# Optimization experiments

Hardware: AMD Instinct MI355X
Metric: run time of the kernel (lower is better)

The kernel has to match this reference:

```python
import jax, jax.numpy as jnp
import numpy as np

N_ = 50000   # nodes
E_ = 800000  # edges
G_ = 64      # graphs in batch
EPS = 1e-5   # batchnorm eps


def _lin(k, fi, fo):
    s = 1.0 / np.sqrt(fi)
    return jax.random.uniform(k, (fi, fo), jnp.float32, -s, s)


def setup_inputs() -> dict:
    key = jax.random.key(0)
    ks = jax.random.split(key, 16)
    d_in, d_h, d_out = 128, 128, 5000
    inp = {
        'x': jax.random.normal(ks[0], (N_, d_in), jnp.float32),
        'edge_index': jax.random.randint(ks[1], (2, E_), 0, N_, jnp.int32),
        'batch': jnp.sort(jax.random.randint(ks[2], (N_,), 0, G_, jnp.int32)),
    }
    dims = [(d_in, d_h), (d_h, d_h), (d_h, d_h), (d_h, d_h)]
    for i, (fi, fo) in enumerate(dims, 1):
        inp[f'w{i}'] = _lin(ks[2 + i], fi, fo)
        inp[f'b{i}'] = jnp.zeros((fo,), jnp.float32)
        inp[f'g{i}'] = jnp.ones((fo,), jnp.float32)   # BN gamma
        inp[f'be{i}'] = jnp.zeros((fo,), jnp.float32)  # BN beta
    inp['gw1'] = _lin(ks[7], d_h, d_h // 2)
    inp['gb1'] = jnp.zeros((d_h // 2,), jnp.float32)
    inp['gw2'] = _lin(ks[8], d_h // 2, 1)
    inp['gb2'] = jnp.zeros((1,), jnp.float32)
    inp['cw'] = _lin(ks[9], d_h, d_out)
    inp['cb'] = jnp.zeros((d_out,), jnp.float32)
    return inp


def reference(x, w1, b1, g1, be1, w2, b2, g2, be2, w3, b3, g3, be3,
              w4, b4, g4, be4, gw1, gb1, gw2, gb2, cw, cb,
              edge_index, batch):
    # GCN normalization with self-loops (PyG GCNConv semantics)
    loops = jnp.arange(N_, dtype=edge_index.dtype)
    src = jnp.concatenate([edge_index[0], loops])
    dst = jnp.concatenate([edge_index[1], loops])
    deg = jax.ops.segment_sum(jnp.ones(src.shape[0], jnp.float32), dst, N_)
    dis = jax.lax.rsqrt(jnp.maximum(deg, 1.0))  # deg >= 1 with self-loops
    norm = dis[src] * dis[dst]                  # [E+N]

    def gcn(h, w, b):
        hw = h @ w                              # [N, d]
        msg = hw[src] * norm[:, None]           # gather over edges
        return jax.ops.segment_sum(msg, dst, N_) + b

    def bn(h, g, be):
        m = h.mean(0)
        v = h.var(0)                            # biased var (training BN)
        return (h - m) * jax.lax.rsqrt(v + EPS) * g + be

    h = x
    for w, b, g, be in ((w1, b1, g1, be1), (w2, b2, g2, be2),
                        (w3, b3, g3, be3), (w4, b4, g4, be4)):
        h = jax.nn.relu(bn(gcn(h, w, b), g, be))  # dropout is identity (eval)

    # attention pooling: per-graph softmax over gate scores
    gate = jax.nn.relu(h @ gw1 + gb1) @ gw2 + gb2  # [N, 1]
    gate = gate[:, 0]
    m = jax.ops.segment_max(gate, batch, G_)
    e = jnp.exp(gate - m[batch])
    s = jax.ops.segment_sum(e, batch, G_)
    a = e / s[batch]                               # [N]
    pooled = jax.ops.segment_sum(h * a[:, None], batch, G_)  # [G, d]
    return pooled @ cw + cb                        # [G, out]
```

## Files before the change

kernel.cpp:

```cpp
#include <hip/hip_runtime.h>
#include <hip/hip_bf16.h>
#include <hip/hip_fp16.h>

#define NN   50000
#define NE   800000
#define NG   64
#define DH   128
#define DOUT 5000
#define BNEPS 1e-5f
#define NBLK 196

typedef _Float16 h8 __attribute__((ext_vector_type(8)));
typedef float    f4 __attribute__((ext_vector_type(4)));

__global__ __launch_bounds__(256) void k_count(const int* __restrict__ dst, int* __restrict__ cnt) {
    int e = blockIdx.x * 256 + threadIdx.x;
    if (e < NE) atomicAdd(&cnt[dst[e]], 1);
}

__global__ __launch_bounds__(256) void k_blkscan(const int* __restrict__ cnt, int* __restrict__ rowptr,
                                                 int* __restrict__ bsum) {
    __shared__ int s[256];
    int t = threadIdx.x, i = blockIdx.x * 256 + t;
    int v = (i < NN) ? cnt[i] : 0;
    s[t] = v;
    __syncthreads();
    for (int off = 1; off < 256; off <<= 1) {
        int x = (t >= off) ? s[t - off] : 0;
        __syncthreads();
        s[t] += x;
        __syncthreads();
    }
    if (i < NN) rowptr[i] = s[t] - v;
    if (t == 255) bsum[blockIdx.x] = s[255];
}

__global__ __launch_bounds__(256) void k_bscan(const int* __restrict__ bsum, int* __restrict__ boff) {
    __shared__ int s[256];
    int t = threadIdx.x;
    int v = (t < NBLK) ? bsum[t] : 0;
    s[t] = v;
    __syncthreads();
    for (int off = 1; off < 256; off <<= 1) {
        int x = (t >= off) ? s[t - off] : 0;
        __syncthreads();
        s[t] += x;
        __syncthreads();
    }
    if (t < NBLK) boff[t] = s[t] - v;
}

__global__ __launch_bounds__(256) void k_fin(int* __restrict__ rowptr, const int* __restrict__ boff,
                                             int* __restrict__ cnt, float* __restrict__ dis) {
    int i = blockIdx.x * 256 + threadIdx.x;
    if (i >= NN) { if (i == NN) rowptr[NN] = NE; return; }
    rowptr[i] += boff[blockIdx.x];
    dis[i] = rsqrtf((float)(cnt[i] + 1));
    cnt[i] = 0;
}

__global__ __launch_bounds__(256) void k_fill(const int* __restrict__ ei, const int* __restrict__ rowptr,
                                              int* __restrict__ fil, const float* __restrict__ dis,
                                              int2* __restrict__ ew) {
    int e = blockIdx.x * 256 + threadIdx.x;
    if (e >= NE) return;
    int s = ei[e], d = ei[NE + e];
    int p = rowptr[d] + atomicAdd(&fil[d], 1);
    ew[p] = make_int2(s, __float_as_int(dis[s] * dis[d]));
}

__global__ __launch_bounds__(256) void k_wprep(const float* __restrict__ W0, const float* __restrict__ W1,
                                               const float* __restrict__ W2, const float* __restrict__ W3,
                                               const float* __restrict__ GW1, __half* __restrict__ Wt) {
    const float* Ws[5] = {W0, W1, W2, W3, GW1};
    int m = blockIdx.x >> 4;
    int chunk = blockIdx.x & 15;
    const float* W = Ws[m];
    __half* O = Wt + m * DH * DH;
    int ncol = (m == 4) ? 64 : DH;
    int total = ncol * DH;
    int o = chunk * 1024 + threadIdx.x;
    for (int r = 0; r < 4; r++, o += 256) {
        if (o < total) {
            int c = o >> 7, k = o & 127;
            O[o] = __float2half(W[k * ncol + c]);
        }
    }
}

__global__ __launch_bounds__(256) void k_gemm3(const float* __restrict__ X, const __half* __restrict__ Wt,
                                               const float* __restrict__ scale, const float* __restrict__ shift,
                                               __half* __restrict__ Y) {
    int t = threadIdx.x;
    int lane = t & 63, wid = t >> 6;
    int wr = wid >> 1, wc = wid & 1;
    int row0 = blockIdx.x * 64;
    int lr = lane & 15, lk = (lane >> 4) * 8;

    f4 acc[2][4];
#pragma unroll
    for (int i = 0; i < 2; i++)
#pragma unroll
        for (int j = 0; j < 4; j++) acc[i][j] = (f4){0.f, 0.f, 0.f, 0.f};

    for (int kt = 0; kt < 4; kt++) {
        int kbase = kt * 32 + lk;
        h8 afr[2];
#pragma unroll
        for (int fr = 0; fr < 2; fr++) {
            int gr = row0 + wr * 32 + fr * 16 + lr;
            gr = min(gr, NN - 1);
            const float4* p = (const float4*)(X + (size_t)gr * DH + kbase);
            float4 v0 = p[0], v1 = p[1];
            if (scale) {
                const float4* sc4 = (const float4*)(scale + kbase);
                const float4* sh4 = (const float4*)(shift + kbase);
                float4 s0 = sc4[0], s1 = sc4[1], h0 = sh4[0], h1 = sh4[1];
                v0.x = fmaxf(fmaf(v0.x, s0.x, h0.x), 0.f);
                v0.y = fmaxf(fmaf(v0.y, s0.y, h0.y), 0.f);
                v0.z = fmaxf(fmaf(v0.z, s0.z, h0.z), 0.f);
                v0.w = fmaxf(fmaf(v0.w, s0.w, h0.w), 0.f);
                v1.x = fmaxf(fmaf(v1.x, s1.x, h1.x), 0.f);
                v1.y = fmaxf(fmaf(v1.y, s1.y, h1.y), 0.f);
                v1.z = fmaxf(fmaf(v1.z, s1.z, h1.z), 0.f);
                v1.w = fmaxf(fmaf(v1.w, s1.w, h1.w), 0.f);
            }
            h8 a;
            a[0] = (_Float16)v0.x; a[1] = (_Float16)v0.y; a[2] = (_Float16)v0.z; a[3] = (_Float16)v0.w;
            a[4] = (_Float16)v1.x; a[5] = (_Float16)v1.y; a[6] = (_Float16)v1.z; a[7] = (_Float16)v1.w;
            afr[fr] = a;
        }
#pragma unroll
        for (int fc = 0; fc < 4; fc++) {
            int gc = wc * 64 + fc * 16 + lr;
            h8 b = *(const h8*)(Wt + (size_t)gc * DH + kbase);
#pragma unroll
            for (int fr = 0; fr < 2; fr++)
                acc[fr][fc] = __builtin_amdgcn_mfma_f32_16x16x32_f16(afr[fr], b, acc[fr][fc], 0, 0, 0);
        }
    }
#pragma unroll
    for (int fr = 0; fr < 2; fr++) {
#pragma unroll
        for (int fc = 0; fc < 4; fc++) {
            int C = wc * 64 + fc * 16 + lr;
#pragma unroll
            for (int q = 0; q < 4; q++) {
                int R = row0 + wr * 32 + fr * 16 + (lane >> 4) * 4 + q;
                if (R < NN) Y[(size_t)R * DH + C] = __float2half(acc[fr][fc][q]);
            }
        }
    }
}

#define EDGE(e) { int2 r = HW4[(size_t)(e).x * 32 + sl]; \
                  float w = __int_as_float((e).y); \
                  float2 g0 = __half22float2(*(__half2*)&r.x), g1 = __half22float2(*(__half2*)&r.y); \
                  a0 = fmaf(w, g0.x, a0); a1 = fmaf(w, g0.y, a1); \
                  a2 = fmaf(w, g1.x, a2); a3 = fmaf(w, g1.y, a3); }

__global__ __launch_bounds__(256) void k_agg(const __half* __restrict__ HW, const int* __restrict__ rowptr,
                                             const int2* __restrict__ EW, const float* __restrict__ dis,
                                             float* __restrict__ OUT,
                                             float* __restrict__ ssum, float* __restrict__ ssq) {
    __shared__ float lsum[DH], lsq[DH];
    int t = threadIdx.x;
    if (t < DH) { lsum[t] = 0.f; lsq[t] = 0.f; }
    __syncthreads();
    int wid = t >> 6, lane = t & 63;
    int sub = lane >> 5, sl = lane & 31;
    const int2* HW4 = (const int2*)HW;
    float4* OUT4 = (float4*)OUT;
    float s0 = 0, s1 = 0, s2 = 0, s3 = 0, q0 = 0, q1 = 0, q2 = 0, q3 = 0;
    int gw = blockIdx.x * 4 + wid;
    for (int i = gw * 2 + sub; i < NN; i += 16384) {
        float sd = dis[i];
        int2 hr = HW4[(size_t)i * 32 + sl];
        float2 f0 = __half22float2(*(__half2*)&hr.x);
        float2 f1 = __half22float2(*(__half2*)&hr.y);
        float wslf = sd * sd;
        float a0 = wslf * f0.x, a1 = wslf * f0.y;
        float a2 = wslf * f1.x, a3 = wslf * f1.y;
        int p = rowptr[i], p1 = rowptr[i + 1];
        for (; p + 8 <= p1; p += 8) {
            int2 e0 = EW[p], e1 = EW[p + 1], e2 = EW[p + 2], e3 = EW[p + 3];
            int2 e4 = EW[p + 4], e5 = EW[p + 5], e6 = EW[p + 6], e7 = EW[p + 7];
            EDGE(e0) EDGE(e1) EDGE(e2) EDGE(e3)
            EDGE(e4) EDGE(e5) EDGE(e6) EDGE(e7)
        }
        if (p + 4 <= p1) {
            int2 e0 = EW[p], e1 = EW[p + 1], e2 = EW[p + 2], e3 = EW[p + 3];
            EDGE(e0) EDGE(e1) EDGE(e2) EDGE(e3)
            p += 4;
        }
        for (; p < p1; p++) {
            int2 e = EW[p];
            EDGE(e)
        }
        OUT4[(size_t)i * 32 + sl] = make_float4(a0, a1, a2, a3);
        s0 += a0; s1 += a1; s2 += a2; s3 += a3;
        q0 += a0 * a0; q1 += a1 * a1; q2 += a2 * a2; q3 += a3 * a3;
    }
    atomicAdd(&lsum[sl * 4 + 0], s0); atomicAdd(&lsum[sl * 4 + 1], s1);
    atomicAdd(&lsum[sl * 4 + 2], s2); atomicAdd(&lsum[sl * 4 + 3], s3);
    atomicAdd(&lsq[sl * 4 + 0], q0);  atomicAdd(&lsq[sl * 4 + 1], q1);
    atomicAdd(&lsq[sl * 4 + 2], q2);  atomicAdd(&lsq[sl * 4 + 3], q3);
    __syncthreads();
    if (t < DH) { atomicAdd(&ssum[t], lsum[t]); atomicAdd(&ssq[t], lsq[t]); }
}

__global__ void k_bnfin(float* __restrict__ ssum, float* __restrict__ ssq,
                        const float* __restrict__ g, const float* __restrict__ be,
                        float* __restrict__ scale, float* __restrict__ shift) {
    int f = threadIdx.x;
    float m = ssum[f] * (1.f / NN);
    float v = ssq[f] * (1.f / NN) - m * m;
    float r = rsqrtf(v + BNEPS);
    float sc = r * g[f];
    scale[f] = sc;
    shift[f] = fmaf(-m, sc, be[f]);
    ssum[f] = 0.f;
    ssq[f] = 0.f;
}

__global__ __launch_bounds__(256) void k_gateM(const float* __restrict__ H, const float* __restrict__ scale,
                                               const float* __restrict__ shift, const __half* __restrict__ gw1t,
                                               const float* __restrict__ gb1, const float* __restrict__ gw2,
                                               const float* __restrict__ gb2, float* __restrict__ gate) {
    int t = threadIdx.x, lane = t & 63, w = t >> 6;
    int row0 = blockIdx.x * 64 + w * 16;
    int lr = lane & 15, lk = (lane >> 4) * 8;
    f4 acc[4];
#pragma unroll
    for (int fc = 0; fc < 4; fc++) acc[fc] = (f4){0.f, 0.f, 0.f, 0.f};

    for (int kt = 0; kt < 4; kt++) {
        int kbase = kt * 32 + lk;
        int gr = min(row0 + lr, NN - 1);
        const float4* p = (const float4*)(H + (size_t)gr * DH + kbase);
        float4 v0 = p[0], v1 = p[1];
        const float4* sc4 = (const float4*)(scale + kbase);
        const float4* sh4 = (const float4*)(shift + kbase);
        float4 s0 = sc4[0], s1 = sc4[1], h0 = sh4[0], h1 = sh4[1];
        v0.x = fmaxf(fmaf(v0.x, s0.x, h0.x), 0.f);
        v0.y = fmaxf(fmaf(v0.y, s0.y, h0.y), 0.f);
        v0.z = fmaxf(fmaf(v0.z, s0.z, h0.z), 0.f);
        v0.w = fmaxf(fmaf(v0.w, s0.w, h0.w), 0.f);
        v1.x = fmaxf(fmaf(v1.x, s1.x, h1.x), 0.f);
        v1.y = fmaxf(fmaf(v1.y, s1.y, h1.y), 0.f);
        v1.z = fmaxf(fmaf(v1.z, s1.z, h1.z), 0.f);
        v1.w = fmaxf(fmaf(v1.w, s1.w, h1.w), 0.f);
        h8 a;
        a[0] = (_Float16)v0.x; a[1] = (_Float16)v0.y; a[2] = (_Float16)v0.z; a[3] = (_Float16)v0.w;
        a[4] = (_Float16)v1.x; a[5] = (_Float16)v1.y; a[6] = (_Float16)v1.z; a[7] = (_Float16)v1.w;
#pragma unroll
        for (int fc = 0; fc < 4; fc++) {
            h8 b = *(const h8*)(gw1t + (size_t)(fc * 16 + lr) * DH + kbase);
            acc[fc] = __builtin_amdgcn_mfma_f32_16x16x32_f16(a, b, acc[fc], 0, 0, 0);
        }
    }
    float vq[4] = {0.f, 0.f, 0.f, 0.f};
#pragma unroll
    for (int fc = 0; fc < 4; fc++) {
        float b1 = gb1[fc * 16 + lr];
        float w2 = gw2[fc * 16 + lr];
#pragma unroll
        for (int q = 0; q < 4; q++)
            vq[q] = fmaf(fmaxf(acc[fc][q] + b1, 0.f), w2, vq[q]);
    }
#pragma unroll
    for (int m = 1; m < 16; m <<= 1) {
#pragma unroll
        for (int q = 0; q < 4; q++) vq[q] += __shfl_xor(vq[q], m, 64);
    }
    if (lr == 0) {
        float b2 = gb2[0];
        int rbase = row0 + (lane >> 4) * 4;
#pragma unroll
        for (int q = 0; q < 4; q++)
            if (rbase + q < NN) gate[rbase + q] = vq[q] + b2;
    }
}

__device__ __forceinline__ int lbound(const int* __restrict__ a, int v) {
    int lo = 0, hi = NN;
    while (lo < hi) {
        int mid = (lo + hi) >> 1;
        if (a[mid] < v) lo = mid + 1; else hi = mid;
    }
    return lo;
}

__global__ __launch_bounds__(256) void k_pms(const float* __restrict__ gate, const int* __restrict__ batch,
                                             float* __restrict__ ms, float* __restrict__ pooled) {
    __shared__ float red[256];
    int g = blockIdx.x, t = threadIdx.x;
    if (t < DH) pooled[g * DH + t] = 0.f;
    int s = lbound(batch, g), e = lbound(batch, g + 1);
    float m = -INFINITY;
    for (int i = s + t; i < e; i += 256) m = fmaxf(m, gate[i]);
    red[t] = m; __syncthreads();
    for (int off = 128; off > 0; off >>= 1) { if (t < off) red[t] = fmaxf(red[t], red[t + off]); __syncthreads(); }
    m = red[0];
    __syncthreads();
    float se = 0.f;
    for (int i = s + t; i < e; i += 256) se += __expf(gate[i] - m);
    red[t] = se; __syncthreads();
    for (int off = 128; off > 0; off >>= 1) { if (t < off) red[t] += red[t + off]; __syncthreads(); }
    if (t == 0) {
        ms[g * 2] = m;
        ms[g * 2 + 1] = (e > s) ? 1.f / red[0] : 0.f;
    }
}

#define PNODES 8
__global__ __launch_bounds__(256) void k_pool2(const float* __restrict__ H, const float* __restrict__ scale,
                                               const float* __restrict__ shift, const float* __restrict__ gate,
                                               const int* __restrict__ batch, const float* __restrict__ ms,
                                               float* __restrict__ pooled) {
    int wid = threadIdx.x >> 6, lane = threadIdx.x & 63;
    int base = (blockIdx.x * 4 + wid) * PNODES;
    if (base >= NN) return;
    int end = min(base + PNODES, NN);
    const float2* H2 = (const float2*)H;
    float2 sc2 = ((const float2*)scale)[lane];
    float2 sh2 = ((const float2*)shift)[lane];
    float2 acc = make_float2(0.f, 0.f);
    int curg = batch[base];
    for (int i = base; i < end; i++) {
        int g = batch[i];
        if (g != curg) {
            atomicAdd(&pooled[curg * DH + lane * 2], acc.x);
            atomicAdd(&pooled[curg * DH + lane * 2 + 1], acc.y);
            acc = make_float2(0.f, 0.f);
            curg = g;
        }
        float a = __expf(gate[i] - ms[g * 2]) * ms[g * 2 + 1];
        float2 h = H2[(size_t)i * 64 + lane];
        float hx = fmaxf(fmaf(h.x, sc2.x, sh2.x), 0.f);
        float hy = fmaxf(fmaf(h.y, sc2.y, sh2.y), 0.f);
        acc.x = fmaf(a, hx, acc.x);
        acc.y = fmaf(a, hy, acc.y);
    }
    atomicAdd(&pooled[curg * DH + lane * 2], acc.x);
    atomicAdd(&pooled[curg * DH + lane * 2 + 1], acc.y);
}

__global__ __launch_bounds__(256) void k_cls(const float* __restrict__ pooled, const float* __restrict__ cw,
                                             const float* __restrict__ cb, float* __restrict__ out) {
    __shared__ float pr[DH];
    int g = blockIdx.y;
    if (threadIdx.x < DH) pr[threadIdx.x] = pooled[g * DH + threadIdx.x];
    __syncthreads();
    int j = blockIdx.x * 256 + threadIdx.x;
    if (j >= DOUT) return;
    float acc = cb[j];
#pragma unroll 8
    for (int k = 0; k < DH; k++) acc = fmaf(pr[k], cw[k * DOUT + j], acc);
    out[g * DOUT + j] = acc;
}

extern "C" void kernel_launch(void* const* d_in, const int* in_sizes, int n_in,
                              void* d_out, int out_size, void* d_ws, size_t ws_size,
                              hipStream_t stream) {
    const float* x     = (const float*)d_in[0];
    const int*   ei    = (const int*)d_in[1];
    const int*   batch = (const int*)d_in[2];
    const float* w[4]  = {(const float*)d_in[3], (const float*)d_in[7], (const float*)d_in[11], (const float*)d_in[15]};
    const float* gg[4] = {(const float*)d_in[5], (const float*)d_in[9], (const float*)d_in[13], (const float*)d_in[17]};
    const float* be[4] = {(const float*)d_in[6], (const float*)d_in[10], (const float*)d_in[14], (const float*)d_in[18]};
    const float* gw1 = (const float*)d_in[19];
    const float* gb1 = (const float*)d_in[20];
    const float* gw2 = (const float*)d_in[21];
    const float* gb2 = (const float*)d_in[22];
    const float* cw  = (const float*)d_in[23];
    const float* cb  = (const float*)d_in[24];

    char* base = (char*)d_ws;
    size_t off = 0;
    auto take = [&](size_t n) -> char* { char* r = base + off; off = (off + n + 255) & ~(size_t)255; return r; };
    float*  bufA   = (float*)take((size_t)NN * DH * 4);
    __half* bufB   = (__half*)take((size_t)NN * DH * 2);
    int2*  ew     = (int2*)take((size_t)NE * 8);
    int*   rowptr = (int*)take((size_t)(NN + 1) * 4);
    int*   cnt    = (int*)take((size_t)NN * 4);
    float* dis    = (float*)take((size_t)NN * 4);
    float* gate   = (float*)take((size_t)NN * 4);
    float* stats  = (float*)take(2 * DH * 4);
    float* ssum = stats, *ssq = stats + DH;
    float* scale  = (float*)take(DH * 4);
    float* shift  = (float*)take(DH * 4);
    float* pooled = (float*)take((size_t)NG * DH * 4);
    int*   bsum   = (int*)take((size_t)256 * 4);
    int*   boff   = (int*)take((size_t)256 * 4);
    float* ms     = (float*)take((size_t)NG * 2 * 4);
    __half* Wt    = (__half*)take((size_t)5 * DH * DH * 2);
    __half* gw1t  = Wt + (size_t)4 * DH * DH;

    hipMemsetAsync(cnt, 0, NN * 4, stream);
    hipMemsetAsync(stats, 0, 2 * DH * 4, stream);
    k_count<<<(NE + 255) / 256, 256, 0, stream>>>(ei + NE, cnt);
    k_blkscan<<<NBLK, 256, 0, stream>>>(cnt, rowptr, bsum);
    k_bscan<<<1, 256, 0, stream>>>(bsum, boff);
    k_fin<<<NBLK, 256, 0, stream>>>(rowptr, boff, cnt, dis);
    k_fill<<<(NE + 255) / 256, 256, 0, stream>>>(ei, rowptr, cnt, dis, ew);
    k_wprep<<<72, 256, 0, stream>>>(w[0], w[1], w[2], w[3], gw1, Wt);

    const int gemm_grid = (NN + 63) / 64;
    for (int L = 0; L < 4; L++) {
        k_gemm3<<<gemm_grid, 256, 0, stream>>>(L == 0 ? x : bufA, Wt + (size_t)L * DH * DH,
                                               L == 0 ? nullptr : scale,
                                               L == 0 ? nullptr : shift, bufB);
        k_agg<<<2048, 256, 0, stream>>>(bufB, rowptr, ew, dis, bufA, ssum, ssq);
        k_bnfin<<<1, DH, 0, stream>>>(ssum, ssq, gg[L], be[L], scale, shift);
    }
    k_gateM<<<(NN + 63) / 64, 256, 0, stream>>>(bufA, scale, shift, gw1t, gb1, gw2, gb2, gate);
    k_pms<<<NG, 256, 0, stream>>>(gate, batch, ms, pooled);
    k_pool2<<<(NN + 4 * PNODES - 1) / (4 * PNODES), 256, 0, stream>>>(bufA, scale, shift, gate, batch, ms, pooled);
    k_cls<<<dim3((DOUT + 255) / 256, NG), 256, 0, stream>>>(pooled, cw, cb, (float*)d_out);
}
```

Baseline: 584.3 us.

## Store aggregated activations in fp16 and fold BN finalize into aggregation kernel

The aggregation output buffer changes from fp32 to fp16, halving the bytes written by k_agg and read by the next layer's GEMM, gate and pooling kernels. The separate one-block BN finalize kernel is removed: the last aggregation block, found with an atomic ticket, computes scale and shift and resets the accumulators. The two memsets are merged into one. This saves launches and memory traffic but adds fp16 rounding of pre-BN activations and a fence-plus-ticket pattern that must be correct.

```diff
diff --git a/kernel.cpp b/kernel.cpp
--- a/kernel.cpp
+++ b/kernel.cpp
@@ -9,6 +9,7 @@
 #define DOUT 5000
 #define BNEPS 1e-5f
 #define NBLK 196
+#define AGG_GRID 2048
 
 typedef _Float16 h8 __attribute__((ext_vector_type(8)));
 typedef float    f4 __attribute__((ext_vector_type(4)));
@@ -88,7 +89,8 @@
     }
 }
 
-__global__ __launch_bounds__(256) void k_gemm3(const float* __restrict__ X, const __half* __restrict__ Wt,
+__global__ __launch_bounds__(256) void k_gemm3(const float* __restrict__ Xf, const __half* __restrict__ Xh,
+                                               const __half* __restrict__ Wt,
                                                const float* __restrict__ scale, const float* __restrict__ shift,
                                                __half* __restrict__ Y) {
     int t = threadIdx.x;
@@ -110,24 +112,31 @@
         for (int fr = 0; fr < 2; fr++) {
             int gr = row0 + wr * 32 + fr * 16 + lr;
             gr = min(gr, NN - 1);
-            const float4* p = (const float4*)(X + (size_t)gr * DH + kbase);
-            float4 v0 = p[0], v1 = p[1];
-            if (scale) {
+            float fv[8];
+            if (Xf) {
+                const float4* p = (const float4*)(Xf + (size_t)gr * DH + kbase);
+                float4 v0 = p[0], v1 = p[1];
+                fv[0] = v0.x; fv[1] = v0.y; fv[2] = v0.z; fv[3] = v0.w;
+                fv[4] = v1.x; fv[5] = v1.y; fv[6] = v1.z; fv[7] = v1.w;
+            } else {
+                int4 hv = *(const int4*)(Xh + (size_t)gr * DH + kbase);
+                float2 p0 = __half22float2(*(__half2*)&hv.x);
+                float2 p1 = __half22float2(*(__half2*)&hv.y);
+                float2 p2 = __half22float2(*(__half2*)&hv.z);
+                float2 p3 = __half22float2(*(__half2*)&hv.w);
+                fv[0] = p0.x; fv[1] = p0.y; fv[2] = p1.x; fv[3] = p1.y;
+                fv[4] = p2.x; fv[5] = p2.y; fv[6] = p3.x; fv[7] = p3.y;
                 const float4* sc4 = (const float4*)(scale + kbase);
                 const float4* sh4 = (const float4*)(shift + kbase);
                 float4 s0 = sc4[0], s1 = sc4[1], h0 = sh4[0], h1 = sh4[1];
-                v0.x = fmaxf(fmaf(v0.x, s0.x, h0.x), 0.f);
-                v0.y = fmaxf(fmaf(v0.y, s0.y, h0.y), 0.f);
-                v0.z = fmaxf(fmaf(v0.z, s0.z, h0.z), 0.f);
-                v0.w = fmaxf(fmaf(v0.w, s0.w, h0.w), 0.f);
-                v1.x = fmaxf(fmaf(v1.x, s1.x, h1.x), 0.f);
-                v1.y = fmaxf(fmaf(v1.y, s1.y, h1.y), 0.f);
-                v1.z = fmaxf(fmaf(v1.z, s1.z, h1.z), 0.f);
-                v1.w = fmaxf(fmaf(v1.w, s1.w, h1.w), 0.f);
+                float sv[8] = {s0.x, s0.y, s0.z, s0.w, s1.x, s1.y, s1.z, s1.w};
+                float hv2[8] = {h0.x, h0.y, h0.z, h0.w, h1.x, h1.y, h1.z, h1.w};
+#pragma unroll
+                for (int j = 0; j < 8; j++) fv[j] = fmaxf(fmaf(fv[j], sv[j], hv2[j]), 0.f);
             }
             h8 a;
-            a[0] = (_Float16)v0.x; a[1] = (_Float16)v0.y; a[2] = (_Float16)v0.z; a[3] = (_Float16)v0.w;
-            a[4] = (_Float16)v1.x; a[5] = (_Float16)v1.y; a[6] = (_Float16)v1.z; a[7] = (_Float16)v1.w;
+#pragma unroll
+            for (int j = 0; j < 8; j++) a[j] = (_Float16)fv[j];
             afr[fr] = a;
         }
 #pragma unroll
@@ -161,8 +170,11 @@
 
 __global__ __launch_bounds__(256) void k_agg(const __half* __restrict__ HW, const int* __restrict__ rowptr,
                                              const int2* __restrict__ EW, const float* __restrict__ dis,
-                                             float* __restrict__ OUT,
-                                             float* __restrict__ ssum, float* __restrict__ ssq) {
+                                             __half* __restrict__ OUT,
+                                             float* __restrict__ ssum, float* __restrict__ ssq,
+                                             const float* __restrict__ gg, const float* __restrict__ be,
+                                             float* __restrict__ scale, float* __restrict__ shift,
+                                             int* __restrict__ ticket) {
     __shared__ float lsum[DH], lsq[DH];
     int t = threadIdx.x;
     if (t < DH) { lsum[t] = 0.f; lsq[t] = 0.f; }
@@ -170,7 +182,6 @@
     int wid = t >> 6, lane = t & 63;
     int sub = lane >> 5, sl = lane & 31;
     const int2* HW4 = (const int2*)HW;
-    float4* OUT4 = (float4*)OUT;
     float s0 = 0, s1 = 0, s2 = 0, s3 = 0, q0 = 0, q1 = 0, q2 = 0, q3 = 0;
     int gw = blockIdx.x * 4 + wid;
     for (int i = gw * 2 + sub; i < NN; i += 16384) {
@@ -197,7 +208,11 @@
             int2 e = EW[p];
             EDGE(e)
         }
-        OUT4[(size_t)i * 32 + sl] = make_float4(a0, a1, a2, a3);
+        __half2 o01 = __floats2half2_rn(a0, a1);
+        __half2 o23 = __floats2half2_rn(a2, a3);
+        int i01 = *(int*)&o01, i23 = *(int*)&o23;
+        long long ov = ((long long)(unsigned)i23 << 32) | (unsigned)i01;
+        *(long long*)(OUT + (size_t)i * DH + sl * 4) = ov;
         s0 += a0; s1 += a1; s2 += a2; s3 += a3;
         q0 += a0 * a0; q1 += a1 * a1; q2 += a2 * a2; q3 += a3 * a3;
     }
@@ -207,23 +222,29 @@
     atomicAdd(&lsq[sl * 4 + 2], q2);  atomicAdd(&lsq[sl * 4 + 3], q3);
     __syncthreads();
     if (t < DH) { atomicAdd(&ssum[t], lsum[t]); atomicAdd(&ssq[t], lsq[t]); }
-}
-
-__global__ void k_bnfin(float* __restrict__ ssum, float* __restrict__ ssq,
-                        const float* __restrict__ g, const float* __restrict__ be,
-                        float* __restrict__ scale, float* __restrict__ shift) {
-    int f = threadIdx.x;
-    float m = ssum[f] * (1.f / NN);
-    float v = ssq[f] * (1.f / NN) - m * m;
-    float r = rsqrtf(v + BNEPS);
-    float sc = r * g[f];
-    scale[f] = sc;
-    shift[f] = fmaf(-m, sc, be[f]);
-    ssum[f] = 0.f;
-    ssq[f] = 0.f;
-}
-
-__global__ __launch_bounds__(256) void k_gateM(const float* __restrict__ H, const float* __restrict__ scale,
+    __syncthreads();
+    __threadfence();
+    __shared__ int lastS;
+    if (t == 0) lastS = (atomicAdd(ticket, 1) == (int)gridDim.x - 1) ? 1 : 0;
+    __syncthreads();
+    if (lastS) {
+        if (t < DH) {
+            float sv = atomicAdd(&ssum[t], 0.f);
+            float qv = atomicAdd(&ssq[t], 0.f);
+            float m = sv * (1.f / NN);
+            float vv = qv * (1.f / NN) - m * m;
+            float r = rsqrtf(vv + BNEPS);
+            float sc = r * gg[t];
+            scale[t] = sc;
+            shift[t] = fmaf(-m, sc, be[t]);
+            ssum[t] = 0.f;
+            ssq[t] = 0.f;
+        }
+        if (t == 0) *ticket = 0;
+    }
+}
+
+__global__ __launch_bounds__(256) void k_gateM(const __half* __restrict__ H, const float* __restrict__ scale,
                                                const float* __restrict__ shift, const __half* __restrict__ gw1t,
                                                const float* __restrict__ gb1, const float* __restrict__ gw2,
                                                const float* __restrict__ gb2, float* __restrict__ gate) {
@@ -237,22 +258,20 @@
     for (int kt = 0; kt < 4; kt++) {
         int kbase = kt * 32 + lk;
         int gr = min(row0 + lr, NN - 1);
-        const float4* p = (const float4*)(H + (size_t)gr * DH + kbase);
-        float4 v0 = p[0], v1 = p[1];
+        int4 hv = *(const int4*)(H + (size_t)gr * DH + kbase);
+        float2 p0 = __half22float2(*(__half2*)&hv.x);
+        float2 p1 = __half22float2(*(__half2*)&hv.y);
+        float2 p2 = __half22float2(*(__half2*)&hv.z);
+        float2 p3 = __half22float2(*(__half2*)&hv.w);
+        float fv[8] = {p0.x, p0.y, p1.x, p1.y, p2.x, p2.y, p3.x, p3.y};
         const float4* sc4 = (const float4*)(scale + kbase);
         const float4* sh4 = (const float4*)(shift + kbase);
         float4 s0 = sc4[0], s1 = sc4[1], h0 = sh4[0], h1 = sh4[1];
-        v0.x = fmaxf(fmaf(v0.x, s0.x, h0.x), 0.f);
-        v0.y = fmaxf(fmaf(v0.y, s0.y, h0.y), 0.f);
-        v0.z = fmaxf(fmaf(v0.z, s0.z, h0.z), 0.f);
-        v0.w = fmaxf(fmaf(v0.w, s0.w, h0.w), 0.f);
-        v1.x = fmaxf(fmaf(v1.x, s1.x, h1.x), 0.f);
-        v1.y = fmaxf(fmaf(v1.y, s1.y, h1.y), 0.f);
-        v1.z = fmaxf(fmaf(v1.z, s1.z, h1.z), 0.f);
-        v1.w = fmaxf(fmaf(v1.w, s1.w, h1.w), 0.f);
+        float sv[8] = {s0.x, s0.y, s0.z, s0.w, s1.x, s1.y, s1.z, s1.w};
+        float hv2[8] = {h0.x, h0.y, h0.z, h0.w, h1.x, h1.y, h1.z, h1.w};
         h8 a;
-        a[0] = (_Float16)v0.x; a[1] = (_Float16)v0.y; a[2] = (_Float16)v0.z; a[3] = (_Float16)v0.w;
-        a[4] = (_Float16)v1.x; a[5] = (_Float16)v1.y; a[6] = (_Float16)v1.z; a[7] = (_Float16)v1.w;
+#pragma unroll
+        for (int j = 0; j < 8; j++) a[j] = (_Float16)fmaxf(fmaf(fv[j], sv[j], hv2[j]), 0.f);
 #pragma unroll
         for (int fc = 0; fc < 4; fc++) {
             h8 b = *(const h8*)(gw1t + (size_t)(fc * 16 + lr) * DH + kbase);
@@ -314,7 +333,7 @@
 }
 
 #define PNODES 8
-__global__ __launch_bounds__(256) void k_pool2(const float* __restrict__ H, const float* __restrict__ scale,
+__global__ __launch_bounds__(256) void k_pool2(const __half* __restrict__ H, const float* __restrict__ scale,
                                                const float* __restrict__ shift, const float* __restrict__ gate,
                                                const int* __restrict__ batch, const float* __restrict__ ms,
                                                float* __restrict__ pooled) {
@@ -322,7 +341,7 @@
     int base = (blockIdx.x * 4 + wid) * PNODES;
     if (base >= NN) return;
     int end = min(base + PNODES, NN);
-    const float2* H2 = (const float2*)H;
+    const __half2* H2 = (const __half2*)H;
     float2 sc2 = ((const float2*)scale)[lane];
     float2 sh2 = ((const float2*)shift)[lane];
     float2 acc = make_float2(0.f, 0.f);
@@ -336,7 +355,7 @@
             curg = g;
         }
         float a = __expf(gate[i] - ms[g * 2]) * ms[g * 2 + 1];
-        float2 h = H2[(size_t)i * 64 + lane];
+        float2 h = __half22float2(H2[(size_t)i * 64 + lane]);
         float hx = fmaxf(fmaf(h.x, sc2.x, sh2.x), 0.f);
         float hy = fmaxf(fmaf(h.y, sc2.y, sh2.y), 0.f);
         acc.x = fmaf(a, hx, acc.x);
@@ -379,15 +398,17 @@
     char* base = (char*)d_ws;
     size_t off = 0;
     auto take = [&](size_t n) -> char* { char* r = base + off; off = (off + n + 255) & ~(size_t)255; return r; };
-    float*  bufA   = (float*)take((size_t)NN * DH * 4);
+    __half* bufA   = (__half*)take((size_t)NN * DH * 2);
     __half* bufB   = (__half*)take((size_t)NN * DH * 2);
     int2*  ew     = (int2*)take((size_t)NE * 8);
     int*   rowptr = (int*)take((size_t)(NN + 1) * 4);
-    int*   cnt    = (int*)take((size_t)NN * 4);
+    char*  zblk   = take((size_t)NN * 4 + 2 * DH * 4 + 64);
+    int*   cnt    = (int*)zblk;
+    float* stats  = (float*)(zblk + (size_t)NN * 4);
+    float* ssum = stats, *ssq = stats + DH;
+    int*   ticket = (int*)(zblk + (size_t)NN * 4 + 2 * DH * 4);
     float* dis    = (float*)take((size_t)NN * 4);
     float* gate   = (float*)take((size_t)NN * 4);
-    float* stats  = (float*)take(2 * DH * 4);
-    float* ssum = stats, *ssq = stats + DH;
     float* scale  = (float*)take(DH * 4);
     float* shift  = (float*)take(DH * 4);
     float* pooled = (float*)take((size_t)NG * DH * 4);
@@ -397,8 +418,7 @@
     __half* Wt    = (__half*)take((size_t)5 * DH * DH * 2);
     __half* gw1t  = Wt + (size_t)4 * DH * DH;
 
-    hipMemsetAsync(cnt, 0, NN * 4, stream);
-    hipMemsetAsync(stats, 0, 2 * DH * 4, stream);
+    hipMemsetAsync(zblk, 0, (size_t)NN * 4 + 2 * DH * 4 + 64, stream);
     k_count<<<(NE + 255) / 256, 256, 0, stream>>>(ei + NE, cnt);
     k_blkscan<<<NBLK, 256, 0, stream>>>(cnt, rowptr, bsum);
     k_bscan<<<1, 256, 0, stream>>>(bsum, boff);
@@ -408,11 +428,12 @@
 
     const int gemm_grid = (NN + 63) / 64;
     for (int L = 0; L < 4; L++) {
-        k_gemm3<<<gemm_grid, 256, 0, stream>>>(L == 0 ? x : bufA, Wt + (size_t)L * DH * DH,
+        k_gemm3<<<gemm_grid, 256, 0, stream>>>(L == 0 ? x : nullptr, L == 0 ? nullptr : bufA,
+                                               Wt + (size_t)L * DH * DH,
                                                L == 0 ? nullptr : scale,
                                                L == 0 ? nullptr : shift, bufB);
-        k_agg<<<2048, 256, 0, stream>>>(bufB, rowptr, ew, dis, bufA, ssum, ssq);
-        k_bnfin<<<1, DH, 0, stream>>>(ssum, ssq, gg[L], be[L], scale, shift);
+        k_agg<<<AGG_GRID, 256, 0, stream>>>(bufB, rowptr, ew, dis, bufA, ssum, ssq,
+                                            gg[L], be[L], scale, shift, ticket);
     }
     k_gateM<<<(NN + 63) / 64, 256, 0, stream>>>(bufA, scale, shift, gw1t, gb1, gw2, gb2, gate);
     k_pms<<<NG, 256, 0, stream>>>(gate, batch, ms, pooled);
```

Result: slower. 867.7 us (+48.5%).
